# Kernel tuning notes

Hardware: AMD Instinct MI355X
Metric: run time of the kernel (lower is better)

Reference implementation:

```python
import jax, jax.numpy as jnp
import numpy as np
import math

WS = 8          # window size
DIM = 32        # per-head dim
NH = 8          # num_head
TH = 16         # total_head
B, H, W = 4, 128, 128
WA = WS * WS    # window area


def _rel_pos_index():
    coords = np.stack(np.meshgrid(np.arange(WS), np.arange(WS), indexing='ij'))  # (2, WS, WS)
    cf = coords.reshape(2, -1)                      # (2, WA)
    rc = cf[:, :, None] - cf[:, None, :]            # (2, WA, WA)
    rc = rc.transpose(1, 2, 0).copy()               # (WA, WA, 2)
    rc[:, :, 0] += WS - 1
    rc[:, :, 1] += WS - 1
    rc[:, :, 0] *= 2 * WS - 1
    return rc.sum(-1)                               # (WA, WA)


def setup_inputs() -> dict:
    key = jax.random.key(0)
    k1, k2, k3, k4 = jax.random.split(key, 4)
    qkv = jax.random.normal(k1, (B, NH, 3 * DIM, H, W), dtype=jnp.float32)
    ch = jax.random.normal(k2, (B, (TH - NH) * DIM, H, W), dtype=jnp.float32)
    logit_scale = jnp.log(10.0) * jnp.ones((NH, 1, 1), dtype=jnp.float32)
    rel_bias_table = 0.02 * jax.random.normal(k3, ((2 * WS - 1) ** 2, NH), dtype=jnp.float32)
    proj_w = 0.02 * jax.random.normal(k4, (NH * DIM, NH * DIM), dtype=jnp.float32)  # 1x1 conv
    proj_b = jnp.zeros((NH * DIM,), dtype=jnp.float32)
    rel_index = jnp.asarray(_rel_pos_index(), dtype=jnp.int32)
    return {"qkv": qkv, "ch": ch, "logit_scale": logit_scale,
            "rel_bias_table": rel_bias_table, "proj_w": proj_w,
            "proj_b": proj_b, "rel_index": rel_index}


def _window_partition(x):
    # x: (B, l, c, H, W) -> (B*nh*nw, l, WA, c)
    b, l, c, h, w = x.shape
    nh, nw = h // WS, w // WS
    x = x.reshape(b, l, c, nh, WS, nw, WS)
    x = x.transpose(0, 3, 5, 1, 4, 6, 2)            # b, nh, nw, l, wh, ww, c
    return x.reshape(b * nh * nw, l, WA, c)


def _l2norm(x):
    n = jnp.sqrt(jnp.sum(x * x, axis=-1, keepdims=True))
    return x / jnp.maximum(n, 1e-12)


def reference(qkv, ch, logit_scale, rel_bias_table, proj_w, proj_b, rel_index):
    b, L, C3, h, w = qkv.shape
    nh, nw = h // WS, w // WS
    qkvw = _window_partition(qkv)                   # (Bw, L, WA, 3*DIM)
    q, k, v = jnp.split(qkvw, 3, axis=-1)           # each (Bw, L, WA, DIM)

    # helper gating
    lch = TH - NH
    chw = _window_partition(ch.reshape(b, lch, DIM, h, w))  # (Bw, lch, WA, DIM)
    chm = jnp.mean(chw, axis=1, keepdims=True)      # (Bw, 1, WA, DIM)
    v = v * chm

    # cosine attention
    attn = jnp.einsum('wlqc,wlkc->wlqk', _l2norm(q), _l2norm(k))
    scale = jnp.exp(jnp.minimum(logit_scale, math.log(1.0 / 0.01)))  # (L,1,1)
    bias = rel_bias_table[rel_index.reshape(-1)].reshape(WA, WA, NH)
    bias = bias.transpose(2, 0, 1)[None]            # (1, L, WA, WA)
    attn = jax.nn.softmax(attn * scale[None] + bias, axis=-1)
    x = jnp.einsum('wlqk,wlkc->wlqc', attn, v)      # (Bw, L, WA, DIM)

    # window unpartition -> (B, L*DIM, H, W)
    x = x.reshape(b, nh, nw, L, WS, WS, DIM)
    x = x.transpose(0, 3, 6, 1, 4, 2, 5)            # b, l, c, nh, wh, nw, ww
    x = x.reshape(b, L * DIM, h, w)

    # 1x1 conv projection
    x = jnp.einsum('bchw,oc->bohw', x, proj_w) + proj_b[None, :, None, None]
    return x
```

## Files before the change

kernel.cpp:

```cpp
#include <hip/hip_runtime.h>
#include <hip/hip_bf16.h>


typedef __attribute__((ext_vector_type(8))) short short8v;
typedef __attribute__((ext_vector_type(4))) float f32x4;
typedef __attribute__((ext_vector_type(4))) unsigned int u32x4;
typedef __attribute__((ext_vector_type(2))) unsigned int u32x2;

#define PLANE 16384
#define LOG100 4.6051701859880914f

static __device__ __forceinline__ unsigned pk2(float a, float b) {
  float2 t; t.x = a; t.y = b;
  __hip_bfloat162 r = __float22bfloat162_rn(t);
  unsigned u;
  __builtin_memcpy(&u, &r, 4);
  return u;
}
struct HiLo { unsigned hi, lo; };
static __device__ __forceinline__ HiLo split2(float x0, float x1) {
  HiLo o;
  o.hi = pk2(x0, x1);
  float h0 = __builtin_bit_cast(float, o.hi << 16);
  float h1 = __builtin_bit_cast(float, o.hi & 0xffff0000u);
  o.lo = pk2(x0 - h0, x1 - h1);
  return o;
}

__global__ __launch_bounds__(256) void prep_kernel(
    const float* __restrict__ ch, const float* __restrict__ btab,
    const int* __restrict__ ridx, const float* __restrict__ pw,
    float* __restrict__ chm, float* __restrict__ biasG,
    unsigned int* __restrict__ wbf)
{
  const int blk = blockIdx.x, tid = threadIdx.x;
  if (blk < 2048) {
    int idx = blk * 256 + tid;
    int b = idx >> 17, c = (idx >> 12) & 31, p4 = idx & 4095;
    const float4* s0 = (const float4*)ch + ((size_t)(b * 256 + c)) * (PLANE / 4) + p4;
    float4 a = {0.f, 0.f, 0.f, 0.f};
#pragma unroll
    for (int l = 0; l < 8; ++l) {
      float4 t = s0[(size_t)(l * 32) * (PLANE / 4)];
      a.x += t.x; a.y += t.y; a.z += t.z; a.w += t.w;
    }
    a.x *= 0.125f; a.y *= 0.125f; a.z *= 0.125f; a.w *= 0.125f;
    ((float4*)chm)[((size_t)(b * 32 + c)) * (PLANE / 4) + p4] = a;
  } else if (blk < 2176) {
    int i = (blk - 2048) * 256 + tid;
    int h = i >> 12, qk = i & 4095;
    biasG[i] = btab[ridx[qk] * 8 + h];
  } else {
    int i = (blk - 2176) * 256 + tid;
    wbf[i] = pk2(pw[2 * i], pw[2 * i + 1]);
  }
}

__global__ __launch_bounds__(256) void fused_kernel(
    const float* __restrict__ qkv, const float* __restrict__ chm,
    const float* __restrict__ lsc, const float* __restrict__ biasG,
    const unsigned short* __restrict__ wbf, const float* __restrict__ pb,
    float* __restrict__ out)
{
  __shared__ __align__(16) char smem[32768];

  const int tid = threadIdx.x;
  const int orig = blockIdx.x;
  const int win = ((orig & 7) << 7) | (orig >> 3);
  const int b  = win >> 8;
  const int wy = (win >> 4) & 15;
  const int wx = win & 15;
  const int y0 = wy << 3, x0 = wx << 3;

  const int wv = tid >> 6, lane = tid & 63;
  const int lg = lane >> 4, lr = lane & 15;

  const float* cg = chm + (size_t)(b * 32) * PLANE;

#pragma unroll 1
  for (int hh = 0; hh < 2; ++hh) {
    const int h = wv + 4 * hh;
    const size_t qbase = ((size_t)((b * 8 + h) * 96)) * PLANE;
    const float* qg = qkv + qbase;
    const float* kg = qg + (size_t)32 * PLANE;
    const float* vg = qg + (size_t)64 * PLANE;
    const float scale = __expf(fminf(lsc[h], LOG100));

    short8v vf[2][2];
#pragma unroll
    for (int dt = 0; dt < 2; ++dt) {
      const int d = 16 * dt + lr;
      const float* vp = vg + (size_t)d * PLANE;
      const float* cp = cg + (size_t)d * PLANE;
#pragma unroll
      for (int m = 0; m < 2; ++m) {
        int ka = 4 * lg + 32 * m, kb = ka + 16;
        int spa = (y0 + (ka >> 3)) * 128 + x0 + (ka & 7);
        int spb = (y0 + (kb >> 3)) * 128 + x0 + (kb & 7);
        float4 va = *(const float4*)(vp + spa);
        float4 ca = *(const float4*)(cp + spa);
        float4 vb = *(const float4*)(vp + spb);
        float4 cb = *(const float4*)(cp + spb);
        u32x4 u;
        u[0] = pk2(va.x * ca.x, va.y * ca.y);
        u[1] = pk2(va.z * ca.z, va.w * ca.w);
        u[2] = pk2(vb.x * cb.x, vb.y * cb.y);
        u[3] = pk2(vb.z * cb.z, vb.w * cb.w);
        vf[dt][m] = __builtin_bit_cast(short8v, u);
      }
    }

    short8v khi[4], klo[4];
#pragma unroll
    for (int kt = 0; kt < 4; ++kt) {
      int kpos = 16 * kt + lr;
      int spk = (y0 + (kpos >> 3)) * 128 + x0 + (kpos & 7);
      float kk[8];
#pragma unroll
      for (int j = 0; j < 8; ++j)
        kk[j] = kg[(size_t)(8 * lg + j) * PLANE + spk];
      float nr = 0.f;
#pragma unroll
      for (int j = 0; j < 8; ++j) nr = fmaf(kk[j], kk[j], nr);
      nr += __shfl_xor(nr, 16);
      nr += __shfl_xor(nr, 32);
      float iv = 1.f / fmaxf(sqrtf(nr), 1e-12f);
      u32x4 uh, ul;
#pragma unroll
      for (int p2 = 0; p2 < 4; ++p2) {
        HiLo hl = split2(kk[2 * p2] * iv, kk[2 * p2 + 1] * iv);
        uh[p2] = hl.hi;
        ul[p2] = hl.lo;
      }
      khi[kt] = __builtin_bit_cast(short8v, uh);
      klo[kt] = __builtin_bit_cast(short8v, ul);
    }

    const float* bgh = biasG + (h << 12);

    float qa[8], qb[8];
    {
      int spq = (y0 + (lr >> 3)) * 128 + x0 + (lr & 7);
#pragma unroll
      for (int j = 0; j < 8; ++j)
        qa[j] = qg[(size_t)(8 * lg + j) * PLANE + spq];
    }
#pragma unroll 1
    for (int st = 0; st < 4; ++st) {
      if (st < 3) {
        int qn = 16 * (st + 1) + lr;
        int spq = (y0 + (qn >> 3)) * 128 + x0 + (qn & 7);
#pragma unroll
        for (int j = 0; j < 8; ++j)
          qb[j] = qg[(size_t)(8 * lg + j) * PLANE + spq];
      }
      const int q = 16 * st + lr;

      float nrq = 0.f;
#pragma unroll
      for (int j = 0; j < 8; ++j) nrq = fmaf(qa[j], qa[j], nrq);
      nrq += __shfl_xor(nrq, 16);
      nrq += __shfl_xor(nrq, 32);
      const float fq = scale / fmaxf(sqrtf(nrq), 1e-12f);

      short8v qhi, qlo;
      {
        u32x4 uh, ul;
#pragma unroll
        for (int p2 = 0; p2 < 4; ++p2) {
          HiLo hl = split2(qa[2 * p2] * fq, qa[2 * p2 + 1] * fq);
          uh[p2] = hl.hi;
          ul[p2] = hl.lo;
        }
        qhi = __builtin_bit_cast(short8v, uh);
        qlo = __builtin_bit_cast(short8v, ul);
      }

      const float4* bq = (const float4*)(bgh + (q << 6));
      float e[16], mx = -1e30f;
      __builtin_amdgcn_s_setprio(1);
#pragma unroll
      for (int kt = 0; kt < 4; ++kt) {
        f32x4 a = {0.f, 0.f, 0.f, 0.f};
        a = __builtin_amdgcn_mfma_f32_16x16x32_bf16(klo[kt], qhi, a, 0, 0, 0);
        a = __builtin_amdgcn_mfma_f32_16x16x32_bf16(khi[kt], qlo, a, 0, 0, 0);
        a = __builtin_amdgcn_mfma_f32_16x16x32_bf16(khi[kt], qhi, a, 0, 0, 0);
        float4 b4 = bq[4 * kt + lg];
        float bb[4] = {b4.x, b4.y, b4.z, b4.w};
#pragma unroll
        for (int r = 0; r < 4; ++r) {
          float lv = a[r] + bb[r];
          e[4 * kt + r] = lv;
          mx = fmaxf(mx, lv);
        }
      }
      __builtin_amdgcn_s_setprio(0);
      mx = fmaxf(mx, __shfl_xor(mx, 16));
      mx = fmaxf(mx, __shfl_xor(mx, 32));
      float s = 0.f;
#pragma unroll
      for (int i = 0; i < 16; ++i) { e[i] = __expf(e[i] - mx); s += e[i]; }
      s += __shfl_xor(s, 16);
      s += __shfl_xor(s, 32);
      float rl = 1.f / s;

      short8v pf[2];
#pragma unroll
      for (int m = 0; m < 2; ++m) {
        u32x4 up;
#pragma unroll
        for (int p2 = 0; p2 < 4; ++p2)
          up[p2] = pk2(e[8 * m + 2 * p2], e[8 * m + 2 * p2 + 1]);
        pf[m] = __builtin_bit_cast(short8v, up);
      }

      const int pl = q;
      __builtin_amdgcn_s_setprio(1);
#pragma unroll
      for (int dt = 0; dt < 2; ++dt) {
        f32x4 o = {0.f, 0.f, 0.f, 0.f};
        o = __builtin_amdgcn_mfma_f32_16x16x32_bf16(vf[dt][0], pf[0], o, 0, 0, 0);
        o = __builtin_amdgcn_mfma_f32_16x16x32_bf16(vf[dt][1], pf[1], o, 0, 0, 0);
        u32x2 ww;
        ww[0] = pk2(o[0] * rl, o[1] * rl);
        ww[1] = pk2(o[2] * rl, o[3] * rl);
        unsigned off = (unsigned)(pl * 512)
                     + (((unsigned)(64 * h + 32 * dt + 8 * lg)) ^ ((unsigned)(pl & 7) << 4));
        *(u32x2*)(smem + off) = ww;
      }
      __builtin_amdgcn_s_setprio(0);

#pragma unroll
      for (int j = 0; j < 8; ++j) qa[j] = qb[j];
    }
  }
  __syncthreads();

  f32x4 acc[4][4];
#pragma unroll
  for (int i = 0; i < 4; ++i)
#pragma unroll
    for (int j = 0; j < 4; ++j) acc[i][j] = (f32x4){0.f, 0.f, 0.f, 0.f};

#pragma unroll 1
  for (int kc = 0; kc < 8; ++kc) {
    short8v wf[4];
#pragma unroll
    for (int ot = 0; ot < 4; ++ot)
      wf[ot] = *(const short8v*)(wbf + (size_t)(64 * wv + 16 * ot + lr) * 256 + 32 * kc + 8 * lg);
    short8v xf[4];
#pragma unroll
    for (int pt = 0; pt < 4; ++pt) {
      int pl = 16 * pt + lr;
      unsigned off = (unsigned)(pl * 512)
                   + (((unsigned)(64 * kc + 16 * lg)) ^ ((unsigned)(pl & 7) << 4));
      xf[pt] = *(const short8v*)(smem + off);
    }
    __builtin_amdgcn_s_setprio(1);
#pragma unroll
    for (int ot = 0; ot < 4; ++ot)
#pragma unroll
      for (int pt = 0; pt < 4; ++pt)
        acc[ot][pt] = __builtin_amdgcn_mfma_f32_16x16x32_bf16(wf[ot], xf[pt], acc[ot][pt], 0, 0, 0);
    __builtin_amdgcn_s_setprio(0);
  }

#pragma unroll
  for (int ot = 0; ot < 4; ++ot) {
#pragma unroll
    for (int r = 0; r < 4; ++r) {
      int o = 64 * wv + 16 * ot + 4 * lg + r;
      float bv = pb[o];
      float* op = out + ((size_t)(b * 256 + o)) * PLANE;
#pragma unroll
      for (int pt = 0; pt < 4; ++pt) {
        int p = 16 * pt + lr;
        op[(y0 + (p >> 3)) * 128 + x0 + (p & 7)] = acc[ot][pt][r] + bv;
      }
    }
  }
}

extern "C" void kernel_launch(void* const* d_in, const int* in_sizes, int n_in,
                              void* d_out, int out_size, void* d_ws, size_t ws_size,
                              hipStream_t stream) {
  const float* qkv  = (const float*)d_in[0];
  const float* ch   = (const float*)d_in[1];
  const float* lsc  = (const float*)d_in[2];
  const float* btab = (const float*)d_in[3];
  const float* pw   = (const float*)d_in[4];
  const float* pb   = (const float*)d_in[5];
  const int*   ridx = (const int*)d_in[6];
  float* out = (float*)d_out;

  char* ws = (char*)d_ws;
  float*          biasG = (float*)ws;
  unsigned short* wbf   = (unsigned short*)(ws + 131072);
  float*          chm   = (float*)(ws + 262144);

  prep_kernel<<<dim3(2304), dim3(256), 0, stream>>>(ch, btab, ridx, pw,
                                                    chm, biasG, (unsigned int*)wbf);
  fused_kernel<<<dim3(1024), dim3(256), 0, stream>>>(qkv, chm, lsc, biasG,
                                                     wbf, pb, out);
}
```

Baseline: 117.3 us.

## Fuse helper-channel mean into attention kernel via shared memory

```diff
diff --git a/kernel.cpp b/kernel.cpp
--- a/kernel.cpp
+++ b/kernel.cpp
@@ -26,43 +26,37 @@
   o.lo = pk2(x0 - h0, x1 - h1);
   return o;
 }
+static __device__ __forceinline__ float lo16f(unsigned u) {
+  return __builtin_bit_cast(float, u << 16);
+}
+static __device__ __forceinline__ float hi16f(unsigned u) {
+  return __builtin_bit_cast(float, u & 0xffff0000u);
+}
 
 __global__ __launch_bounds__(256) void prep_kernel(
-    const float* __restrict__ ch, const float* __restrict__ btab,
-    const int* __restrict__ ridx, const float* __restrict__ pw,
-    float* __restrict__ chm, float* __restrict__ biasG,
+    const float* __restrict__ btab, const int* __restrict__ ridx,
+    const float* __restrict__ pw, float* __restrict__ biasG,
     unsigned int* __restrict__ wbf)
 {
   const int blk = blockIdx.x, tid = threadIdx.x;
-  if (blk < 2048) {
-    int idx = blk * 256 + tid;
-    int b = idx >> 17, c = (idx >> 12) & 31, p4 = idx & 4095;
-    const float4* s0 = (const float4*)ch + ((size_t)(b * 256 + c)) * (PLANE / 4) + p4;
-    float4 a = {0.f, 0.f, 0.f, 0.f};
-#pragma unroll
-    for (int l = 0; l < 8; ++l) {
-      float4 t = s0[(size_t)(l * 32) * (PLANE / 4)];
-      a.x += t.x; a.y += t.y; a.z += t.z; a.w += t.w;
-    }
-    a.x *= 0.125f; a.y *= 0.125f; a.z *= 0.125f; a.w *= 0.125f;
-    ((float4*)chm)[((size_t)(b * 32 + c)) * (PLANE / 4) + p4] = a;
-  } else if (blk < 2176) {
-    int i = (blk - 2048) * 256 + tid;
+  if (blk < 128) {
+    int i = blk * 256 + tid;
     int h = i >> 12, qk = i & 4095;
     biasG[i] = btab[ridx[qk] * 8 + h];
   } else {
-    int i = (blk - 2176) * 256 + tid;
+    int i = (blk - 128) * 256 + tid;
     wbf[i] = pk2(pw[2 * i], pw[2 * i + 1]);
   }
 }
 
 __global__ __launch_bounds__(256) void fused_kernel(
-    const float* __restrict__ qkv, const float* __restrict__ chm,
+    const float* __restrict__ qkv, const float* __restrict__ ch,
     const float* __restrict__ lsc, const float* __restrict__ biasG,
     const unsigned short* __restrict__ wbf, const float* __restrict__ pb,
     float* __restrict__ out)
 {
   __shared__ __align__(16) char smem[32768];
+  __shared__ __align__(8) unsigned short chms[32][72];
 
   const int tid = threadIdx.x;
   const int orig = blockIdx.x;
@@ -75,7 +69,29 @@
   const int wv = tid >> 6, lane = tid & 63;
   const int lg = lane >> 4, lr = lane & 15;
 
-  const float* cg = chm + (size_t)(b * 32) * PLANE;
+  {
+    const float* cb = ch + ((size_t)(b * 256)) * PLANE;
+#pragma unroll
+    for (int t = 0; t < 2; ++t) {
+      int idx = tid + (t << 8);
+      int c = idx >> 4, u = idx & 15;
+      int row = u >> 1, xh = u & 1;
+      const float4* src = (const float4*)(cb + (size_t)c * PLANE
+                                          + (y0 + row) * 128 + x0 + 4 * xh);
+      float4 a = {0.f, 0.f, 0.f, 0.f};
+#pragma unroll
+      for (int l = 0; l < 8; ++l) {
+        float4 tv = src[(size_t)(l * 32) * (PLANE / 4)];
+        a.x += tv.x; a.y += tv.y; a.z += tv.z; a.w += tv.w;
+      }
+      a.x *= 0.125f; a.y *= 0.125f; a.z *= 0.125f; a.w *= 0.125f;
+      u32x2 pk;
+      pk[0] = pk2(a.x, a.y);
+      pk[1] = pk2(a.z, a.w);
+      *(u32x2*)(&chms[c][4 * u]) = pk;
+    }
+  }
+  __syncthreads();
 
 #pragma unroll 1
   for (int hh = 0; hh < 2; ++hh) {
@@ -91,21 +107,21 @@
     for (int dt = 0; dt < 2; ++dt) {
       const int d = 16 * dt + lr;
       const float* vp = vg + (size_t)d * PLANE;
-      const float* cp = cg + (size_t)d * PLANE;
+      const unsigned short* cmr = &chms[d][0];
 #pragma unroll
       for (int m = 0; m < 2; ++m) {
         int ka = 4 * lg + 32 * m, kb = ka + 16;
         int spa = (y0 + (ka >> 3)) * 128 + x0 + (ka & 7);
         int spb = (y0 + (kb >> 3)) * 128 + x0 + (kb & 7);
         float4 va = *(const float4*)(vp + spa);
-        float4 ca = *(const float4*)(cp + spa);
         float4 vb = *(const float4*)(vp + spb);
-        float4 cb = *(const float4*)(cp + spb);
+        u32x2 ca = *(const u32x2*)(cmr + ka);
+        u32x2 cb2 = *(const u32x2*)(cmr + kb);
         u32x4 u;
-        u[0] = pk2(va.x * ca.x, va.y * ca.y);
-        u[1] = pk2(va.z * ca.z, va.w * ca.w);
-        u[2] = pk2(vb.x * cb.x, vb.y * cb.y);
-        u[3] = pk2(vb.z * cb.z, vb.w * cb.w);
+        u[0] = pk2(va.x * lo16f(ca[0]), va.y * hi16f(ca[0]));
+        u[1] = pk2(va.z * lo16f(ca[1]), va.w * hi16f(ca[1]));
+        u[2] = pk2(vb.x * lo16f(cb2[0]), vb.y * hi16f(cb2[0]));
+        u[3] = pk2(vb.z * lo16f(cb2[1]), vb.w * hi16f(cb2[1]));
         vf[dt][m] = __builtin_bit_cast(short8v, u);
       }
     }
@@ -296,10 +312,9 @@
   char* ws = (char*)d_ws;
   float*          biasG = (float*)ws;
   unsigned short* wbf   = (unsigned short*)(ws + 131072);
-  float*          chm   = (float*)(ws + 262144);
-
-  prep_kernel<<<dim3(2304), dim3(256), 0, stream>>>(ch, btab, ridx, pw,
-                                                    chm, biasG, (unsigned int*)wbf);
-  fused_kernel<<<dim3(1024), dim3(256), 0, stream>>>(qkv, chm, lsc, biasG,
+
+  prep_kernel<<<dim3(256), dim3(256), 0, stream>>>(btab, ridx, pw,
+                                                   biasG, (unsigned int*)wbf);
+  fused_kernel<<<dim3(1024), dim3(256), 0, stream>>>(qkv, ch, lsc, biasG,
                                                      wbf, pb, out);
 }
```

Result: slower. 149.4 us (+27.3%).
